# Performance work log

Measured on AMD Instinct MI355X. Metric: run time of the kernel, lower is better.

The kernel has to match this reference:

```python
import jax, jax.numpy as jnp
import numpy as np

IN_DIM, D_MODEL, HIDDEN, N_BLOCKS, N_CLASSES = 784, 16, 6, 4, 10
BATCH = 65536


def setup_inputs() -> dict:
    key = jax.random.key(0)
    ks = jax.random.split(key, 6)
    std = 0.02
    x = jax.random.normal(ks[0], (BATCH, IN_DIM), dtype=jnp.float32)
    # nn.Linear stores weight as [out, in]; we keep that convention.
    W_embed = jax.random.normal(ks[1], (D_MODEL, IN_DIM), dtype=jnp.float32) * std
    L_w = jax.random.normal(ks[2], (N_BLOCKS, HIDDEN, D_MODEL), dtype=jnp.float32) * std
    R_w = jax.random.normal(ks[3], (N_BLOCKS, HIDDEN, D_MODEL), dtype=jnp.float32) * std
    D_w = jax.random.normal(ks[4], (N_BLOCKS, D_MODEL, HIDDEN), dtype=jnp.float32) * std
    W_head = jax.random.normal(ks[5], (N_CLASSES, D_MODEL), dtype=jnp.float32) * std
    return {"x": x, "W_embed": W_embed, "L_w": L_w, "R_w": R_w, "D_w": D_w, "W_head": W_head}


def reference(x, W_embed, L_w, R_w, D_w, W_head):
    # embed: [B, in_dim] @ [in_dim, d_model]
    h_x = x @ W_embed.T  # [B, d_model]
    all_h = []
    for i in range(N_BLOCKS):  # n_blocks is a small structural constant
        u = h_x @ L_w[i].T  # [B, hidden]
        v = h_x @ R_w[i].T  # [B, hidden]
        h = u * v
        h_x = h_x + h @ D_w[i].T  # residual
        all_h.append(h)
    logits = h_x @ W_head.T  # [B, n_classes]
    return (logits, *all_h)
```

## Files before the change

kernel.cpp:

```cpp
#include <hip/hip_runtime.h>


#define IN_DIM   784
#define D_MODEL  16
#define HIDDEN   6
#define N_BLOCKS 4
#define N_CLS    10
#define BATCH    65536
#define NCHUNK   12

typedef const __attribute__((address_space(1))) void gvoid_t;
typedef __attribute__((address_space(3))) void svoid_t;

__global__ __launch_bounds__(512, 8) void bilinear_resnet_fused(
    const float* __restrict__ x,
    const float* __restrict__ W_embed,
    const float* __restrict__ L_w,
    const float* __restrict__ R_w,
    const float* __restrict__ D_w,
    const float* __restrict__ W_head,
    float* __restrict__ out)
{
    __shared__ float4 buf[2][64 * 16];

    const int tid  = threadIdx.x;
    const int lane = tid & 63;
    const int wv   = __builtin_amdgcn_readfirstlane(tid >> 6);
    const int row  = blockIdx.x * 64 + lane;
    const float* xtile = x + (size_t)blockIdx.x * 64 * IN_DIM;

    const int rhalf = tid >> 4;
    const int kk_l  = (tid & 15) ^ (rhalf & 15);

    const float2 xtail = *reinterpret_cast<const float2*>(
        x + (size_t)row * IN_DIM + 768 + wv * 2);

    float acc[D_MODEL];
#pragma unroll
    for (int d = 0; d < D_MODEL; ++d) acc[d] = 0.f;

    auto stage = [&](int k, int b) {
#pragma unroll
        for (int it = 0; it < 2; ++it) {
            const int r = it * 32 + rhalf;
            const float* g = xtile + (size_t)r * IN_DIM + k * 64 + kk_l * 4;
            char* l = (char*)(&buf[b][0]) + (it * 512 + tid) * 16;
            __builtin_amdgcn_global_load_lds((gvoid_t*)g, (svoid_t*)l, 16, 0, 0);
        }
    };

    auto compute = [&](int c, int b) {
        const float* wc = W_embed + c * 64 + wv * 8;
        const float4* bsrc = buf[b];
#pragma unroll
        for (int j = 0; j < 2; ++j) {
            const int kk = wv * 2 + j;
            const float4 xv = bsrc[lane * 16 + (kk ^ (lane & 15))];
#pragma unroll
            for (int d = 0; d < D_MODEL; ++d) {
                const float* wd = wc + d * IN_DIM + j * 4;
                float s = acc[d];
                s = fmaf(xv.x, wd[0], s);
                s = fmaf(xv.y, wd[1], s);
                s = fmaf(xv.z, wd[2], s);
                s = fmaf(xv.w, wd[3], s);
                acc[d] = s;
            }
        }
    };

    stage(0, 0);
    __syncthreads();

    for (int c = 0; c < NCHUNK; ++c) {
        if (c + 1 < NCHUNK) stage(c + 1, (c + 1) & 1);
        compute(c, c & 1);
        __syncthreads();
    }

    {
        const float* wt = W_embed + 768 + wv * 2;
#pragma unroll
        for (int d = 0; d < D_MODEL; ++d) {
            const float* wd = wt + d * IN_DIM;
            acc[d] = fmaf(xtail.x, wd[0], fmaf(xtail.y, wd[1], acc[d]));
        }
    }

    float* parts = reinterpret_cast<float*>(&buf[0][0]);
    if (wv != 0) {
#pragma unroll
        for (int d = 0; d < D_MODEL; ++d)
            parts[((wv - 1) * 64 + lane) * 17 + d] = acc[d];
    }
    __syncthreads();
    if (wv != 0) return;

#pragma unroll
    for (int p = 0; p < 7; ++p)
#pragma unroll
        for (int d = 0; d < D_MODEL; ++d)
            acc[d] += parts[(p * 64 + lane) * 17 + d];

#pragma unroll
    for (int b = 0; b < N_BLOCKS; ++b) {
        const float* Lb = L_w + b * HIDDEN * D_MODEL;
        const float* Rb = R_w + b * HIDDEN * D_MODEL;
        const float* Db = D_w + b * D_MODEL * HIDDEN;
        float h[HIDDEN];
#pragma unroll
        for (int j = 0; j < HIDDEN; ++j) {
            float u = 0.f, v = 0.f;
#pragma unroll
            for (int d = 0; d < D_MODEL; ++d) {
                u = fmaf(acc[d], Lb[j * D_MODEL + d], u);
                v = fmaf(acc[d], Rb[j * D_MODEL + d], v);
            }
            h[j] = u * v;
        }
#pragma unroll
        for (int d = 0; d < D_MODEL; ++d) {
            float s = acc[d];
#pragma unroll
            for (int j = 0; j < HIDDEN; ++j) s = fmaf(h[j], Db[d * HIDDEN + j], s);
            acc[d] = s;
        }
        float* hout = out + (size_t)N_CLS * BATCH + (size_t)b * HIDDEN * BATCH
                      + (size_t)row * HIDDEN;
#pragma unroll
        for (int j = 0; j < HIDDEN; ++j) hout[j] = h[j];
    }

    float* lout = out + (size_t)row * N_CLS;
#pragma unroll
    for (int k = 0; k < N_CLS; ++k) {
        float s = 0.f;
#pragma unroll
        for (int d = 0; d < D_MODEL; ++d) s = fmaf(acc[d], W_head[k * D_MODEL + d], s);
        lout[k] = s;
    }
}

extern "C" void kernel_launch(void* const* d_in, const int* in_sizes, int n_in,
                              void* d_out, int out_size, void* d_ws, size_t ws_size,
                              hipStream_t stream) {
    const float* x       = (const float*)d_in[0];
    const float* W_embed = (const float*)d_in[1];
    const float* L_w     = (const float*)d_in[2];
    const float* R_w     = (const float*)d_in[3];
    const float* D_w     = (const float*)d_in[4];
    const float* W_head  = (const float*)d_in[5];
    float* out = (float*)d_out;

    const int grid = BATCH / 64;
    bilinear_resnet_fused<<<grid, 512, 0, stream>>>(
        x, W_embed, L_w, R_w, D_w, W_head, out);
}
```

Measured before the change: 329.5 us.

## Replace LDS-staged embed GEMM with per-thread row streaming over direct global loads

Drops the double-buffered global_load_lds staging of x tiles. Each thread now handles one row and 4 output columns, streaming float4 loads of x and W_embed straight from global memory across the full 784-wide dot product. Blocks shrink from 512 to 256 threads, and the cross-wave partial-sum reduction is replaced by a single LDS transpose. Access to x becomes row-strided per lane, four lanes share a row, and the x loads are uncoalesced across rows. This risks poorer memory efficiency in exchange for less synchronisation and simpler code.

Result: slower. 585.4 us (+77.6%).

```diff
diff --git a/kernel.cpp b/kernel.cpp
--- a/kernel.cpp
+++ b/kernel.cpp
@@ -7,12 +7,9 @@
 #define N_BLOCKS 4
 #define N_CLS    10
 #define BATCH    65536
-#define NCHUNK   12
+#define NT       196
 
-typedef const __attribute__((address_space(1))) void gvoid_t;
-typedef __attribute__((address_space(3))) void svoid_t;
-
-__global__ __launch_bounds__(512, 8) void bilinear_resnet_fused(
+__global__ __launch_bounds__(256, 4) void bilinear_resnet_fused(
     const float* __restrict__ x,
     const float* __restrict__ W_embed,
     const float* __restrict__ L_w,
@@ -21,86 +18,49 @@
     const float* __restrict__ W_head,
     float* __restrict__ out)
 {
-    __shared__ float4 buf[2][64 * 16];
+    __shared__ float accLDS[64][17];
 
     const int tid  = threadIdx.x;
     const int lane = tid & 63;
-    const int wv   = __builtin_amdgcn_readfirstlane(tid >> 6);
-    const int row  = blockIdx.x * 64 + lane;
-    const float* xtile = x + (size_t)blockIdx.x * 64 * IN_DIM;
+    const int wv   = tid >> 6;
+    const int rloc = lane >> 2;
+    const int phi  = lane & 3;
+    const int rb   = wv * 16 + rloc;
+    const int row  = blockIdx.x * 64 + rb;
 
-    const int rhalf = tid >> 4;
-    const int kk_l  = (tid & 15) ^ (rhalf & 15);
+    const float* xr = x + (size_t)row * IN_DIM;
+    const float* wr0 = W_embed + (size_t)(phi * 4 + 0) * IN_DIM;
+    const float* wr1 = W_embed + (size_t)(phi * 4 + 1) * IN_DIM;
+    const float* wr2 = W_embed + (size_t)(phi * 4 + 2) * IN_DIM;
+    const float* wr3 = W_embed + (size_t)(phi * 4 + 3) * IN_DIM;
 
-    const float2 xtail = *reinterpret_cast<const float2*>(
-        x + (size_t)row * IN_DIM + 768 + wv * 2);
+    float a0 = 0.f, a1 = 0.f, a2 = 0.f, a3 = 0.f;
+
+#pragma unroll 4
+    for (int t = 0; t < NT; ++t) {
+        const float4 xv = *reinterpret_cast<const float4*>(xr  + 4 * t);
+        const float4 w0 = *reinterpret_cast<const float4*>(wr0 + 4 * t);
+        const float4 w1 = *reinterpret_cast<const float4*>(wr1 + 4 * t);
+        const float4 w2 = *reinterpret_cast<const float4*>(wr2 + 4 * t);
+        const float4 w3 = *reinterpret_cast<const float4*>(wr3 + 4 * t);
+        a0 = fmaf(xv.w, w0.w, fmaf(xv.z, w0.z, fmaf(xv.y, w0.y, fmaf(xv.x, w0.x, a0))));
+        a1 = fmaf(xv.w, w1.w, fmaf(xv.z, w1.z, fmaf(xv.y, w1.y, fmaf(xv.x, w1.x, a1))));
+        a2 = fmaf(xv.w, w2.w, fmaf(xv.z, w2.z, fmaf(xv.y, w2.y, fmaf(xv.x, w2.x, a2))));
+        a3 = fmaf(xv.w, w3.w, fmaf(xv.z, w3.z, fmaf(xv.y, w3.y, fmaf(xv.x, w3.x, a3))));
+    }
+
+    accLDS[rb][phi * 4 + 0] = a0;
+    accLDS[rb][phi * 4 + 1] = a1;
+    accLDS[rb][phi * 4 + 2] = a2;
+    accLDS[rb][phi * 4 + 3] = a3;
+    __syncthreads();
+    if (wv != 0) return;
 
     float acc[D_MODEL];
 #pragma unroll
-    for (int d = 0; d < D_MODEL; ++d) acc[d] = 0.f;
+    for (int d = 0; d < D_MODEL; ++d) acc[d] = accLDS[lane][d];
 
-    auto stage = [&](int k, int b) {
-#pragma unroll
-        for (int it = 0; it < 2; ++it) {
-            const int r = it * 32 + rhalf;
-            const float* g = xtile + (size_t)r * IN_DIM + k * 64 + kk_l * 4;
-            char* l = (char*)(&buf[b][0]) + (it * 512 + tid) * 16;
-            __builtin_amdgcn_global_load_lds((gvoid_t*)g, (svoid_t*)l, 16, 0, 0);
-        }
-    };
-
-    auto compute = [&](int c, int b) {
-        const float* wc = W_embed + c * 64 + wv * 8;
-        const float4* bsrc = buf[b];
-#pragma unroll
-        for (int j = 0; j < 2; ++j) {
-            const int kk = wv * 2 + j;
-            const float4 xv = bsrc[lane * 16 + (kk ^ (lane & 15))];
-#pragma unroll
-            for (int d = 0; d < D_MODEL; ++d) {
-                const float* wd = wc + d * IN_DIM + j * 4;
-                float s = acc[d];
-                s = fmaf(xv.x, wd[0], s);
-                s = fmaf(xv.y, wd[1], s);
-                s = fmaf(xv.z, wd[2], s);
-                s = fmaf(xv.w, wd[3], s);
-                acc[d] = s;
-            }
-        }
-    };
-
-    stage(0, 0);
-    __syncthreads();
-
-    for (int c = 0; c < NCHUNK; ++c) {
-        if (c + 1 < NCHUNK) stage(c + 1, (c + 1) & 1);
-        compute(c, c & 1);
-        __syncthreads();
-    }
-
-    {
-        const float* wt = W_embed + 768 + wv * 2;
-#pragma unroll
-        for (int d = 0; d < D_MODEL; ++d) {
-            const float* wd = wt + d * IN_DIM;
-            acc[d] = fmaf(xtail.x, wd[0], fmaf(xtail.y, wd[1], acc[d]));
-        }
-    }
-
-    float* parts = reinterpret_cast<float*>(&buf[0][0]);
-    if (wv != 0) {
-#pragma unroll
-        for (int d = 0; d < D_MODEL; ++d)
-            parts[((wv - 1) * 64 + lane) * 17 + d] = acc[d];
-    }
-    __syncthreads();
-    if (wv != 0) return;
-
-#pragma unroll
-    for (int p = 0; p < 7; ++p)
-#pragma unroll
-        for (int d = 0; d < D_MODEL; ++d)
-            acc[d] += parts[(p * 64 + lane) * 17 + d];
+    const int erow = blockIdx.x * 64 + lane;
 
 #pragma unroll
     for (int b = 0; b < N_BLOCKS; ++b) {
@@ -126,12 +86,12 @@
             acc[d] = s;
         }
         float* hout = out + (size_t)N_CLS * BATCH + (size_t)b * HIDDEN * BATCH
-                      + (size_t)row * HIDDEN;
+                      + (size_t)erow * HIDDEN;
 #pragma unroll
         for (int j = 0; j < HIDDEN; ++j) hout[j] = h[j];
     }
 
-    float* lout = out + (size_t)row * N_CLS;
+    float* lout = out + (size_t)erow * N_CLS;
 #pragma unroll
     for (int k = 0; k < N_CLS; ++k) {
         float s = 0.f;
@@ -153,6 +113,6 @@
     float* out = (float*)d_out;
 
     const int grid = BATCH / 64;
-    bilinear_resnet_fused<<<grid, 512, 0, stream>>>(
+    bilinear_resnet_fused<<<grid, 256, 0, stream>>>(
         x, W_embed, L_w, R_w, D_w, W_head, out);
 }
```
